# Performance work log

Hardware: AMD Instinct MI355X
Metric: run time of the kernel (lower is better)

## Reference

```python
import jax, jax.numpy as jnp
import numpy as np

LEAKY_ALPHA = 0.2  # tf.nn.leaky_relu default

N_NODES = 65536
N_EDGES = 1048576
D = 64


def setup_inputs() -> dict:
    key = jax.random.key(0)
    k1, k2, k3, k4 = jax.random.split(key, 4)
    x = jax.random.normal(k1, (N_NODES, D), dtype=jnp.float32)
    edge_index = jax.random.randint(k2, (2, N_EDGES), 0, N_NODES, dtype=jnp.int64)
    W1 = jax.random.normal(k3, (D, D), dtype=jnp.float32) * 0.05
    b1 = jnp.zeros((D,), dtype=jnp.float32)
    W2 = jax.random.normal(k4, (D, D), dtype=jnp.float32) * 0.05
    b2 = jnp.zeros((D,), dtype=jnp.float32)
    return {"x": x, "edge_index": edge_index, "W1": W1, "b1": b1, "W2": W2, "b2": b2}


def _leaky_relu(v):
    return jnp.where(v >= 0, v, LEAKY_ALPHA * v)


def reference(x, edge_index, W1, b1, W2, b2):
    n = x.shape[0]
    src = edge_index[0]
    dst = edge_index[1]
    # LightGCN symmetric normalization: w_e = deg[src]^-1/2 * deg[dst]^-1/2
    ones = jnp.ones(src.shape, dtype=x.dtype)
    deg = jax.ops.segment_sum(ones, dst, num_segments=n)
    inv_sqrt = jnp.where(deg > 0, jax.lax.rsqrt(jnp.maximum(deg, 1.0)), 0.0)
    w = inv_sqrt[src] * inv_sqrt[dst]  # [E]
    # SpMM: h = normed_adj @ x  (gather + weighted scatter-add)
    h = jax.ops.segment_sum(x[src] * w[:, None], dst, num_segments=n)  # [N, D]
    # dual dense transform + elementwise gate
    out = _leaky_relu(h @ W1 + b1) + _leaky_relu((x * h) @ W2 + b2)
    return out
```

## Files before the change

kernel.cpp:

```cpp
#include <hip/hip_runtime.h>

#define N_NODES 65536
#define N_EDGES 1048576
#define D 64
#define NB 256
#define CHUNK (N_EDGES / NB)
#define SSTAGE 6144
#define FBCAP 65536

typedef __bf16 bf16x8 __attribute__((ext_vector_type(8)));
typedef float f32x4 __attribute__((ext_vector_type(4)));

__device__ __forceinline__ int edge_at(const void* ei, int is64, long long pos) {
    if (is64) return (int)((const long long*)ei)[pos];
    return ((const int*)ei)[pos];
}

__device__ __forceinline__ int detect_is64(const unsigned* ei, int* s_is64) {
    if (threadIdx.x < 64) {
        unsigned v = ei[2 * threadIdx.x + 1];
        unsigned long long nz = __ballot(v != 0u);
        if (threadIdx.x == 0) *s_is64 = (nz == 0ull) ? 1 : 0;
    }
    __syncthreads();
    return *s_is64;
}

__global__ __launch_bounds__(256) void passA_kernel(const void* ei,
                                                    unsigned* __restrict__ H,
                                                    unsigned* __restrict__ L,
                                                    unsigned* __restrict__ pairs_cs) {
    __shared__ unsigned ed[CHUNK];
    __shared__ unsigned srt[CHUNK];
    __shared__ unsigned hist[NB];
    __shared__ unsigned scn[NB];
    __shared__ int s_is64;
    const int is64 = detect_is64((const unsigned*)ei, &s_is64);
    const int t = threadIdx.x;
    const int w = blockIdx.x;
    hist[t] = 0;
    __syncthreads();
    const int base = w * CHUNK;
    for (int i = t; i < CHUNK; i += 256) {
        unsigned src = (unsigned)edge_at(ei, is64, base + i);
        unsigned dst = (unsigned)edge_at(ei, is64, (long long)N_EDGES + base + i);
        ed[i] = src | (dst << 16);
        atomicAdd(&hist[dst >> 8], 1u);
    }
    __syncthreads();
    const unsigned own = hist[t];
    scn[t] = own;
    __syncthreads();
    for (int off = 1; off < NB; off <<= 1) {
        unsigned v = (t >= off) ? scn[t - off] : 0u;
        __syncthreads();
        scn[t] += v;
        __syncthreads();
    }
    const unsigned excl = scn[t] - own;
    H[t * NB + w] = own;
    L[t * NB + w] = excl;
    hist[t] = excl;
    __syncthreads();
    for (int i = t; i < CHUNK; i += 256) {
        unsigned p = ed[i];
        unsigned pos = atomicAdd(&hist[p >> 24], 1u);
        srt[pos] = p;
    }
    __syncthreads();
    for (int i = t; i < CHUNK; i += 256) pairs_cs[(size_t)w * CHUNK + i] = srt[i];
}

__global__ __launch_bounds__(256) void bucketB_kernel(const unsigned* __restrict__ pairs_cs,
                                                      const unsigned* __restrict__ H,
                                                      const unsigned* __restrict__ L,
                                                      const float* __restrict__ x,
                                                      unsigned* __restrict__ row_start,
                                                      unsigned short* __restrict__ src16,
                                                      unsigned* __restrict__ y32,
                                                      unsigned* __restrict__ fb) {
    __shared__ unsigned s_pairs[SSTAGE];
    __shared__ unsigned short s_src[SSTAGE];
    __shared__ unsigned hist[NB];
    __shared__ unsigned scn[NB];
    __shared__ unsigned degs[NB];
    __shared__ unsigned s_tot[NB];
    const int t = threadIdx.x;
    const int b = blockIdx.x;

    {
        const uint4* Hr = (const uint4*)(H + t * NB);
        unsigned tt = 0;
#pragma unroll 8
        for (int k = 0; k < NB / 4; ++k) {
            uint4 q = Hr[k];
            tt += q.x + q.y + q.z + q.w;
        }
        s_tot[t] = tt;
        scn[t] = tt;
    }
    __syncthreads();
    for (int off = 1; off < NB; off <<= 1) {
        unsigned v = (t >= off) ? scn[t - off] : 0u;
        __syncthreads();
        scn[t] += v;
        __syncthreads();
    }
    const unsigned base = scn[b] - s_tot[b];
    const unsigned cnt = s_tot[b];
    const bool staged = (cnt <= SSTAGE);
    __syncthreads();

    const unsigned Hb = H[b * NB + t];
    const unsigned Lb = L[b * NB + t];
    scn[t] = Hb;
    __syncthreads();
    for (int off = 1; off < NB; off <<= 1) {
        unsigned v = (t >= off) ? scn[t - off] : 0u;
        __syncthreads();
        scn[t] += v;
        __syncthreads();
    }
    const unsigned ex = scn[t] - Hb;
    unsigned* wp = staged ? s_pairs : (fb + (size_t)b * FBCAP);
    for (unsigned j = 0; j < Hb; ++j) wp[ex + j] = pairs_cs[(size_t)t * CHUNK + Lb + j];
    __syncthreads();
    const unsigned* pp = staged ? s_pairs : (fb + (size_t)b * FBCAP);

    hist[t] = 0;
    __syncthreads();
    for (unsigned i = t; i < cnt; i += 256u) {
        atomicAdd(&hist[(pp[i] >> 16) & 255u], 1u);
    }
    __syncthreads();
    const unsigned own = hist[t];
    degs[t] = own;
    scn[t] = own;
    __syncthreads();
    for (int off = 1; off < NB; off <<= 1) {
        unsigned v = (t >= off) ? scn[t - off] : 0u;
        __syncthreads();
        scn[t] += v;
        __syncthreads();
    }
    const unsigned excl = scn[t] - own;
    row_start[b * NB + t] = base + excl;
    if (b == NB - 1 && t == 0) row_start[N_NODES] = N_EDGES;
    hist[t] = excl;
    __syncthreads();
    if (staged) {
        for (unsigned i = t; i < cnt; i += 256u) {
            unsigned p = pp[i];
            unsigned pos = atomicAdd(&hist[(p >> 16) & 255u], 1u);
            s_src[pos] = (unsigned short)(p & 0xFFFFu);
        }
        __syncthreads();
        for (unsigned i = t; i < cnt; i += 256u) src16[base + i] = s_src[i];
    } else {
        for (unsigned i = t; i < cnt; i += 256u) {
            unsigned p = pp[i];
            unsigned pos = atomicAdd(&hist[(p >> 16) & 255u], 1u);
            src16[base + pos] = (unsigned short)(p & 0xFFFFu);
        }
    }
    const int nbase = b * NB;
    for (int idx = t; idx < NB * 32; idx += 256) {
        int nl = idx >> 5;
        int col = idx & 31;
        unsigned d = degs[nl];
        float w = d ? rsqrtf((float)d) : 0.f;
        float2 v = *(const float2*)(x + (nbase + nl) * D + col * 2);
        unsigned lo = (unsigned)__builtin_bit_cast(unsigned short, (__bf16)(v.x * w));
        unsigned hi = (unsigned)__builtin_bit_cast(unsigned short, (__bf16)(v.y * w));
        y32[(size_t)(nbase + nl) * 32 + col] = lo | (hi << 16);
    }
}

#define BLO(u) __uint_as_float((u) << 16)
#define BHI(u) __uint_as_float((u) & 0xffff0000u)
__device__ __forceinline__ unsigned pkbf(float lo, float hi) {
    return (unsigned)__builtin_bit_cast(unsigned short, (__bf16)lo) |
           ((unsigned)__builtin_bit_cast(unsigned short, (__bf16)hi) << 16);
}
__device__ __forceinline__ void acc8(uint4 p, float* a) {
    a[0] += BLO(p.x); a[1] += BHI(p.x);
    a[2] += BLO(p.y); a[3] += BHI(p.y);
    a[4] += BLO(p.z); a[5] += BHI(p.z);
    a[6] += BLO(p.w); a[7] += BHI(p.w);
}
__global__ __launch_bounds__(256) void spmm_kernel(const unsigned short* __restrict__ src16,
                                                   const unsigned* __restrict__ row_start,
                                                   const uint4* __restrict__ y128,
                                                   uint4* __restrict__ hb4) {
    const int lane = threadIdx.x & 63;
    const int g = lane >> 3;
    const int r8 = lane & 7;
    int wv = (blockIdx.x * blockDim.x + threadIdx.x) >> 6;
    int nwv = (gridDim.x * blockDim.x) >> 6;
    for (int nb = wv * 8; nb < N_NODES; nb += nwv * 8) {
        const int n = nb + g;
        const unsigned start = row_start[n];
        const unsigned end = row_start[n + 1];
        float a[8] = {0.f, 0.f, 0.f, 0.f, 0.f, 0.f, 0.f, 0.f};
        float c[8] = {0.f, 0.f, 0.f, 0.f, 0.f, 0.f, 0.f, 0.f};
        unsigned i = start;
        for (; i + 4 <= end; i += 4) {
            int s0 = (int)src16[i];
            int s1 = (int)src16[i + 1];
            int s2 = (int)src16[i + 2];
            int s3 = (int)src16[i + 3];
            uint4 p0 = y128[s0 * 8 + r8];
            uint4 p1 = y128[s1 * 8 + r8];
            uint4 p2 = y128[s2 * 8 + r8];
            uint4 p3 = y128[s3 * 8 + r8];
            acc8(p0, a); acc8(p1, c);
            acc8(p2, a); acc8(p3, c);
        }
        for (; i < end; ++i) {
            uint4 p = y128[(int)src16[i] * 8 + r8];
            acc8(p, a);
        }
        const float w = (end > start) ? rsqrtf((float)(end - start)) : 0.f;
        uint4 v;
        v.x = pkbf((a[0] + c[0]) * w, (a[1] + c[1]) * w);
        v.y = pkbf((a[2] + c[2]) * w, (a[3] + c[3]) * w);
        v.z = pkbf((a[4] + c[4]) * w, (a[5] + c[5]) * w);
        v.w = pkbf((a[6] + c[6]) * w, (a[7] + c[7]) * w);
        hb4[(size_t)nb * 8 + lane] = v;
    }
}

__global__ __launch_bounds__(256) void dense_mfma_kernel(const uint4* __restrict__ y128,
                                                         const uint4* __restrict__ hb4,
                                                         const unsigned* __restrict__ row_start,
                                                         const float* __restrict__ W1,
                                                         const float* __restrict__ b1,
                                                         const float* __restrict__ W2,
                                                         const float* __restrict__ b2,
                                                         float* __restrict__ out) {
    const int lane = threadIdx.x & 63;
    const int lo = lane & 15;
    const int hi = lane >> 4;

    bf16x8 bw1[2][4], bw2[2][4];
#pragma unroll
    for (int kt = 0; kt < 2; ++kt)
#pragma unroll
        for (int nt = 0; nt < 4; ++nt) {
            bf16x8 v1, v2;
#pragma unroll
            for (int j = 0; j < 8; ++j) {
                int k = kt * 32 + hi * 8 + j;
                int n = nt * 16 + lo;
                v1[j] = (__bf16)W1[k * D + n];
                v2[j] = (__bf16)W2[k * D + n];
            }
            bw1[kt][nt] = v1;
            bw2[kt][nt] = v2;
        }
    float bb1[4], bb2[4];
#pragma unroll
    for (int nt = 0; nt < 4; ++nt) {
        bb1[nt] = b1[nt * 16 + lo];
        bb2[nt] = b2[nt * 16 + lo];
    }

    int wid = (blockIdx.x * blockDim.x + threadIdx.x) >> 6;
    int nw = (gridDim.x * blockDim.x) >> 6;
    for (int blk = wid; blk < N_NODES / 16; blk += nw) {
        const int rb = blk * 16;
        const int row = rb + lo;
        const uint4* hrow = hb4 + (size_t)row * 8;
        const uint4* yrow = y128 + (size_t)row * 8;
        const float sd = sqrtf((float)(row_start[row + 1] - row_start[row]));
        bf16x8 ah[2], ag[2];
#pragma unroll
        for (int kt = 0; kt < 2; ++kt) {
            uint4 hp = hrow[kt * 4 + hi];
            uint4 yp = yrow[kt * 4 + hi];
            ah[kt] = __builtin_bit_cast(bf16x8, hp);
            bf16x8 g;
            g[0] = (__bf16)(BLO(hp.x) * (BLO(yp.x) * sd));
            g[1] = (__bf16)(BHI(hp.x) * (BHI(yp.x) * sd));
            g[2] = (__bf16)(BLO(hp.y) * (BLO(yp.y) * sd));
            g[3] = (__bf16)(BHI(hp.y) * (BHI(yp.y) * sd));
            g[4] = (__bf16)(BLO(hp.z) * (BLO(yp.z) * sd));
            g[5] = (__bf16)(BHI(hp.z) * (BHI(yp.z) * sd));
            g[6] = (__bf16)(BLO(hp.w) * (BLO(yp.w) * sd));
            g[7] = (__bf16)(BHI(hp.w) * (BHI(yp.w) * sd));
            ag[kt] = g;
        }
        f32x4 acc1[4], acc2[4];
#pragma unroll
        for (int nt = 0; nt < 4; ++nt) {
            acc1[nt] = (f32x4){0.f, 0.f, 0.f, 0.f};
            acc2[nt] = (f32x4){0.f, 0.f, 0.f, 0.f};
        }
#pragma unroll
        for (int kt = 0; kt < 2; ++kt)
#pragma unroll
            for (int nt = 0; nt < 4; ++nt) {
                acc1[nt] = __builtin_amdgcn_mfma_f32_16x16x32_bf16(ah[kt], bw1[kt][nt], acc1[nt], 0, 0, 0);
                acc2[nt] = __builtin_amdgcn_mfma_f32_16x16x32_bf16(ag[kt], bw2[kt][nt], acc2[nt], 0, 0, 0);
            }
#pragma unroll
        for (int nt = 0; nt < 4; ++nt)
#pragma unroll
            for (int r = 0; r < 4; ++r) {
                float a1 = acc1[nt][r] + bb1[nt];
                float a2 = acc2[nt][r] + bb2[nt];
                a1 = (a1 >= 0.f) ? a1 : 0.2f * a1;
                a2 = (a2 >= 0.f) ? a2 : 0.2f * a2;
                out[(rb + hi * 4 + r) * D + nt * 16 + lo] = a1 + a2;
            }
    }
}

extern "C" void kernel_launch(void* const* d_in, const int* in_sizes, int n_in,
                              void* d_out, int out_size, void* d_ws, size_t ws_size,
                              hipStream_t stream) {
    const float* x  = (const float*)d_in[0];
    const void*  ei = d_in[1];
    const float* W1 = (const float*)d_in[2];
    const float* b1 = (const float*)d_in[3];
    const float* W2 = (const float*)d_in[4];
    const float* b2 = (const float*)d_in[5];
    float* out = (float*)d_out;

    char* p = (char*)d_ws;
    unsigned* row_start    = (unsigned*)p;       p += 266240;
    unsigned* H            = (unsigned*)p;       p += NB * NB * 4;
    unsigned* L            = (unsigned*)p;       p += NB * NB * 4;
    unsigned short* src16  = (unsigned short*)p; p += (size_t)N_EDGES * 2;
    unsigned* y32          = (unsigned*)p;       p += (size_t)N_NODES * 32 * 4;
    unsigned* hb           = (unsigned*)p;       p += (size_t)N_NODES * 32 * 4;
    unsigned* fb           = (unsigned*)p;

    unsigned* pairs_cs = (unsigned*)d_out;

    passA_kernel<<<NB, 256, 0, stream>>>(ei, H, L, pairs_cs);
    bucketB_kernel<<<NB, 256, 0, stream>>>(pairs_cs, H, L, x, row_start, src16, y32, fb);
    spmm_kernel<<<2048, 256, 0, stream>>>(src16, row_start, (const uint4*)y32, (uint4*)hb);
    dense_mfma_kernel<<<1024, 256, 0, stream>>>((const uint4*)y32, (const uint4*)hb,
                                                row_start, W1, b1, W2, b2, out);
}
```

Before: 71.84 us.

## Balance bucket gather via binary search and split y scaling into own kernel

The gather of per-chunk runs into each bucket used to be a serial per-thread copy loop of variable length. It now has each thread handle strided output elements and find the source run by binary search over run offsets, so the work is spread evenly and reads are more coalesced. The x-to-bf16 scaling by inverse sqrt degree moves out of bucketB into a separate fully parallel y_kernel that reads degrees from row_start. This adds one kernel launch and a small extra read of row_start, but shortens bucketB's tail.

```diff
diff --git a/kernel.cpp b/kernel.cpp
--- a/kernel.cpp
+++ b/kernel.cpp
@@ -74,17 +74,16 @@
 __global__ __launch_bounds__(256) void bucketB_kernel(const unsigned* __restrict__ pairs_cs,
                                                       const unsigned* __restrict__ H,
                                                       const unsigned* __restrict__ L,
-                                                      const float* __restrict__ x,
                                                       unsigned* __restrict__ row_start,
                                                       unsigned short* __restrict__ src16,
-                                                      unsigned* __restrict__ y32,
                                                       unsigned* __restrict__ fb) {
     __shared__ unsigned s_pairs[SSTAGE];
     __shared__ unsigned short s_src[SSTAGE];
     __shared__ unsigned hist[NB];
     __shared__ unsigned scn[NB];
-    __shared__ unsigned degs[NB];
     __shared__ unsigned s_tot[NB];
+    __shared__ unsigned s_runoff[NB + 1];
+    __shared__ unsigned s_Lb[NB];
     const int t = threadIdx.x;
     const int b = blockIdx.x;
 
@@ -112,7 +111,7 @@
     __syncthreads();
 
     const unsigned Hb = H[b * NB + t];
-    const unsigned Lb = L[b * NB + t];
+    s_Lb[t] = L[b * NB + t];
     scn[t] = Hb;
     __syncthreads();
     for (int off = 1; off < NB; off <<= 1) {
@@ -121,9 +120,19 @@
         scn[t] += v;
         __syncthreads();
     }
-    const unsigned ex = scn[t] - Hb;
+    s_runoff[t] = scn[t] - Hb;
+    if (t == NB - 1) s_runoff[NB] = scn[t];
+    __syncthreads();
+
     unsigned* wp = staged ? s_pairs : (fb + (size_t)b * FBCAP);
-    for (unsigned j = 0; j < Hb; ++j) wp[ex + j] = pairs_cs[(size_t)t * CHUNK + Lb + j];
+    for (unsigned i = t; i < cnt; i += 256u) {
+        int lo2 = 0, hi2 = NB;
+        while (hi2 - lo2 > 1) {
+            int mid = (lo2 + hi2) >> 1;
+            if (s_runoff[mid] <= i) lo2 = mid; else hi2 = mid;
+        }
+        wp[i] = pairs_cs[(size_t)lo2 * CHUNK + s_Lb[lo2] + (i - s_runoff[lo2])];
+    }
     __syncthreads();
     const unsigned* pp = staged ? s_pairs : (fb + (size_t)b * FBCAP);
 
@@ -134,7 +143,6 @@
     }
     __syncthreads();
     const unsigned own = hist[t];
-    degs[t] = own;
     scn[t] = own;
     __syncthreads();
     for (int off = 1; off < NB; off <<= 1) {
@@ -163,17 +171,20 @@
             src16[base + pos] = (unsigned short)(p & 0xFFFFu);
         }
     }
-    const int nbase = b * NB;
-    for (int idx = t; idx < NB * 32; idx += 256) {
-        int nl = idx >> 5;
-        int col = idx & 31;
-        unsigned d = degs[nl];
-        float w = d ? rsqrtf((float)d) : 0.f;
-        float2 v = *(const float2*)(x + (nbase + nl) * D + col * 2);
-        unsigned lo = (unsigned)__builtin_bit_cast(unsigned short, (__bf16)(v.x * w));
-        unsigned hi = (unsigned)__builtin_bit_cast(unsigned short, (__bf16)(v.y * w));
-        y32[(size_t)(nbase + nl) * 32 + col] = lo | (hi << 16);
-    }
+}
+
+__global__ __launch_bounds__(256) void y_kernel(const float* __restrict__ x,
+                                                const unsigned* __restrict__ row_start,
+                                                unsigned* __restrict__ y32) {
+    int idx = blockIdx.x * blockDim.x + threadIdx.x;
+    int n = idx >> 5;
+    int col = idx & 31;
+    unsigned d = row_start[n + 1] - row_start[n];
+    float w = d ? rsqrtf((float)d) : 0.f;
+    float2 v = *(const float2*)(x + n * D + col * 2);
+    unsigned lo = (unsigned)__builtin_bit_cast(unsigned short, (__bf16)(v.x * w));
+    unsigned hi = (unsigned)__builtin_bit_cast(unsigned short, (__bf16)(v.y * w));
+    y32[idx] = lo | (hi << 16);
 }
 
 #define BLO(u) __uint_as_float((u) << 16)
@@ -339,7 +350,8 @@
     unsigned* pairs_cs = (unsigned*)d_out;
 
     passA_kernel<<<NB, 256, 0, stream>>>(ei, H, L, pairs_cs);
-    bucketB_kernel<<<NB, 256, 0, stream>>>(pairs_cs, H, L, x, row_start, src16, y32, fb);
+    bucketB_kernel<<<NB, 256, 0, stream>>>(pairs_cs, H, L, row_start, src16, fb);
+    y_kernel<<<N_NODES * 32 / 256, 256, 0, stream>>>(x, row_start, y32);
     spmm_kernel<<<2048, 256, 0, stream>>>(src16, row_start, (const uint4*)y32, (uint4*)hb);
     dense_mfma_kernel<<<1024, 256, 0, stream>>>((const uint4*)y32, (const uint4*)hb,
                                                 row_start, W1, b1, W2, b2, out);
```

Result: slower. 80.25 us (+11.7%).
